# Performance work log

Measured on AMD Instinct MI355X. Metric: run time of the kernel, lower is better.

## Reference

```python
import jax, jax.numpy as jnp
import numpy as np

N = 100000      # nodes
E = 1600000     # edges (avg degree 16)
IN = 128        # in_size
H = 4           # num_heads
DH = 16         # hid_size (per-head)
DO = 16         # out_size (per-head)
NEG_SLOPE = 0.2 # DGL GATConv default leaky_relu slope


def setup_inputs():
    key = jax.random.key(0)
    ks = jax.random.split(key, 12)
    s = 0.1
    return {
        "x":   jax.random.normal(ks[0], (N, IN), jnp.float32),
        "src": jax.random.randint(ks[1], (E,), 0, N, jnp.int32),
        "dst": jax.random.randint(ks[2], (E,), 0, N, jnp.int32),
        # layer 1: in=128 -> H*DH=64, residual Linear (128 != 64)
        "W1":    jax.random.normal(ks[3], (IN, H * DH), jnp.float32) * s,
        "al1":   jax.random.normal(ks[4], (H, DH), jnp.float32) * s,
        "ar1":   jax.random.normal(ks[5], (H, DH), jnp.float32) * s,
        "resW1": jax.random.normal(ks[6], (IN, H * DH), jnp.float32) * s,
        "b1":    jnp.zeros((H * DH,), jnp.float32),
        # layer 2: in=H*DH=64 -> H*DO=64, residual is Identity reshape (64 == 64)
        "W2":  jax.random.normal(ks[7], (H * DH, H * DO), jnp.float32) * s,
        "al2": jax.random.normal(ks[8], (H, DO), jnp.float32) * s,
        "ar2": jax.random.normal(ks[9], (H, DO), jnp.float32) * s,
        "b2":  jnp.zeros((H * DO,), jnp.float32),
    }


def gat_layer(h, W, al, ar, res, bias, src, dst):
    """One DGL-style GATConv (no internal activation). Returns [N, H, D]."""
    d = W.shape[1] // H
    feat = (h @ W).reshape(-1, H, d)                       # [N,H,D]
    el = jnp.einsum('nhd,hd->nh', feat, al)                # [N,H]
    er = jnp.einsum('nhd,hd->nh', feat, ar)                # [N,H]
    e = jax.nn.leaky_relu(el[src] + er[dst], NEG_SLOPE)    # [E,H]
    # segment softmax over incoming edges of each destination node
    emax = jax.lax.stop_gradient(jax.ops.segment_max(e, dst, num_segments=N))
    ee = jnp.exp(e - emax[dst])                            # [E,H]
    den = jax.ops.segment_sum(ee, dst, num_segments=N)     # [N,H]
    alpha = ee / den[dst]                                  # [E,H]
    msg = alpha[:, :, None] * feat[src]                    # [E,H,D]
    out = jax.ops.segment_sum(msg, dst, num_segments=N)    # [N,H,D]
    return out + res + bias.reshape(1, H, d)


def reference(x, src, dst, W1, al1, ar1, resW1, b1, W2, al2, ar2, b2):
    # layer 1 (residual via Linear since IN != H*DH)
    res1 = (x @ resW1).reshape(N, H, DH)
    h = gat_layer(x, W1, al1, ar1, res1, b1, src, dst)     # [N,H,DH]
    h = jax.nn.elu(h.reshape(N, H * DH))                   # flatten + elu (dropout=eval identity)
    # layer 2 (identity residual since H*DH == H*DO)
    res2 = h.reshape(N, H, DO)
    h = gat_layer(h, W2, al2, ar2, res2, b2, src, dst)     # [N,H,DO]
    return h.mean(axis=1)                                  # [N,DO]
```

## Files before the change

### kernel.cpp

```cpp
#include <hip/hip_runtime.h>
#include <hip/hip_bf16.h>

static inline int cdiv(int a, int b){ return (a+b-1)/b; }

#define LEAKY(x) ((x) >= 0.f ? (x) : 0.2f*(x))

#define NBK   512
#define NBKSH 9
#define CAP   12288

__device__ inline unsigned short bf16bits(float f){
  __hip_bfloat16 h = __float2bfloat16(f);
  return *reinterpret_cast<unsigned short*>(&h);
}


__global__ __launch_bounds__(256) void binA(const int* __restrict__ src,
    const int* __restrict__ dst, int* __restrict__ acur, unsigned int* __restrict__ tmp,
    int E, int B, int epb)
{
  __shared__ int cnt1[256], cnt2[256], gbase[256];
  const int tid = threadIdx.x;
  cnt1[tid] = 0; cnt2[tid] = 0;
  __syncthreads();
  const int beg = blockIdx.x*epb, end = min(E, beg+epb);
  for (int e = beg+tid; e < end; e += 256) atomicAdd(&cnt1[dst[e]>>NBKSH], 1);
  __syncthreads();
  if (tid < B) gbase[tid] = atomicAdd(&acur[tid], cnt1[tid]);
  __syncthreads();
  for (int e = beg+tid; e < end; e += 256) {
    int s = src[e], d = dst[e];
    int b = d >> NBKSH;
    int tk = atomicAdd(&cnt2[b], 1);
    int slot = gbase[b] + tk;
    if (slot < CAP)
      tmp[(size_t)b*CAP + slot] = ((unsigned)s << NBKSH) | (unsigned)(d & (NBK-1));
  }
}


__global__ __launch_bounds__(256) void bucket_scan(const int* __restrict__ acur,
    int* __restrict__ bbase, int* __restrict__ off, int B, int N, int E)
{
  __shared__ int wsum[4];
  const int tid = threadIdx.x, lane = tid & 63, wave = tid >> 6;
  int v = (tid < B) ? acur[tid] : 0;
  int x = v;
  #pragma unroll
  for (int s = 1; s < 64; s <<= 1) { int t = __shfl_up(x, s); if (lane >= s) x += t; }
  if (lane == 63) wsum[wave] = x;
  __syncthreads();
  if (tid == 0) { int r = 0; for (int w = 0; w < 4; w++) { int t = wsum[w]; wsum[w] = r; r += t; } }
  __syncthreads();
  int excl = wsum[wave] + x - v;
  if (tid < B)    bbase[tid] = excl;
  if (tid == B-1) bbase[B]   = excl + v;
  if (tid == 0)   off[N]     = E;
}


__global__ __launch_bounds__(256) void binC(const unsigned int* __restrict__ tmp,
    const int* __restrict__ acur, const int* __restrict__ bbase,
    int* __restrict__ off, int* __restrict__ csr_src, int N)
{
  __shared__ int sA[NBK], sB[NBK];
  const int b = blockIdx.x, tid = threadIdx.x;
  const int m = min(acur[b], CAP);
  const int base = bbase[b];
  const int n0 = b*NBK;
  const int nn = min(NBK, N - n0);
  for (int j = tid; j < NBK; j += 256) sA[j] = 0;
  __syncthreads();
  const unsigned int* tb = tmp + (size_t)b*CAP;
  for (int i = tid; i < m; i += 256) atomicAdd(&sA[tb[i] & (NBK-1)], 1);
  __syncthreads();
  int* in = sA; int* ob = sB;
  for (int st = 1; st < NBK; st <<= 1) {
    for (int j = tid; j < NBK; j += 256) { int v = in[j]; if (j >= st) v += in[j-st]; ob[j] = v; }
    __syncthreads();
    int* t = in; in = ob; ob = t;
  }
  for (int j = tid; j < NBK; j += 256) ob[j] = j ? in[j-1] : 0;
  __syncthreads();
  for (int j = tid; j < nn; j += 256) off[n0 + j] = base + ob[j];
  __syncthreads();
  for (int i = tid; i < m; i += 256) {
    unsigned v = tb[i];
    int pos = atomicAdd(&ob[v & (NBK-1)], 1);
    csr_src[base + pos] = (int)(v >> NBKSH);
  }
}


template<bool ATTN, bool BF16OUT>
__global__ __launch_bounds__(256) void lin128(const float* __restrict__ X,
    const float* __restrict__ W, const float* __restrict__ al, const float* __restrict__ ar,
    void* __restrict__ featout, float* __restrict__ el, float* __restrict__ er, int n)
{
  __shared__ float Ws[128*64];
  __shared__ float Xs[32*129];
  const int tid = threadIdx.x;
  const int nbase = blockIdx.x * 32;
  for (int i = tid; i < 128*64/4; i += 256) ((float4*)Ws)[i] = ((const float4*)W)[i];
  for (int idx = tid; idx < 32*32; idx += 256) {
    int node = idx >> 5, fq = idx & 31;
    int gn = nbase + node;
    float4 v = (gn < n) ? ((const float4*)X)[(size_t)gn*32 + fq] : float4{0.f,0.f,0.f,0.f};
    Xs[node*129 + fq*4 + 0] = v.x;
    Xs[node*129 + fq*4 + 1] = v.y;
    Xs[node*129 + fq*4 + 2] = v.z;
    Xs[node*129 + fq*4 + 3] = v.w;
  }
  __syncthreads();
  const int c0 = (tid & 15) * 4;
  const int n0 = (tid >> 4) * 2;
  float a00=0,a01=0,a02=0,a03=0, a10=0,a11=0,a12=0,a13=0;
  #pragma unroll 4
  for (int k = 0; k < 128; k++) {
    float4 w = *(const float4*)&Ws[k*64 + c0];
    float x0 = Xs[n0*129 + k];
    float x1 = Xs[n0*129 + 129 + k];
    a00 = fmaf(x0, w.x, a00); a01 = fmaf(x0, w.y, a01);
    a02 = fmaf(x0, w.z, a02); a03 = fmaf(x0, w.w, a03);
    a10 = fmaf(x1, w.x, a10); a11 = fmaf(x1, w.y, a11);
    a12 = fmaf(x1, w.z, a12); a13 = fmaf(x1, w.w, a13);
  }
  const int g0 = nbase + n0, g1 = g0 + 1;
  if (BF16OUT) {
    unsigned short* fb = (unsigned short*)featout;
    if (g0 < n) *(ushort4*)&fb[(size_t)g0*64 + c0] = ushort4{bf16bits(a00),bf16bits(a01),bf16bits(a02),bf16bits(a03)};
    if (g1 < n) *(ushort4*)&fb[(size_t)g1*64 + c0] = ushort4{bf16bits(a10),bf16bits(a11),bf16bits(a12),bf16bits(a13)};
  } else {
    float* fb = (float*)featout;
    if (g0 < n) *(float4*)&fb[(size_t)g0*64 + c0] = float4{a00,a01,a02,a03};
    if (g1 < n) *(float4*)&fb[(size_t)g1*64 + c0] = float4{a10,a11,a12,a13};
  }
  if (ATTN) {
    float l0=al[c0], l1=al[c0+1], l2=al[c0+2], l3=al[c0+3];
    float r0=ar[c0], r1=ar[c0+1], r2=ar[c0+2], r3=ar[c0+3];
    float e0 = a00*l0 + a01*l1 + a02*l2 + a03*l3;
    float e1 = a10*l0 + a11*l1 + a12*l2 + a13*l3;
    float q0 = a00*r0 + a01*r1 + a02*r2 + a03*r3;
    float q1 = a10*r0 + a11*r1 + a12*r2 + a13*r3;
    e0 += __shfl_xor(e0,1); e0 += __shfl_xor(e0,2);
    e1 += __shfl_xor(e1,1); e1 += __shfl_xor(e1,2);
    q0 += __shfl_xor(q0,1); q0 += __shfl_xor(q0,2);
    q1 += __shfl_xor(q1,1); q1 += __shfl_xor(q1,2);
    if ((tid & 3) == 0) {
      int h = (tid & 15) >> 2;
      if (g0 < n) { el[g0*4+h] = e0; er[g0*4+h] = q0; }
      if (g1 < n) { el[g1*4+h] = e1; er[g1*4+h] = q1; }
    }
  }
}


__global__ __launch_bounds__(256) void lin64(const float* __restrict__ X,
    const float* __restrict__ W, const float* __restrict__ al, const float* __restrict__ ar,
    unsigned short* __restrict__ feat, float* __restrict__ el, float* __restrict__ er, int n)
{
  __shared__ float Ws[64*64];
  __shared__ float Xs[64*65];
  const int tid = threadIdx.x;
  const int nbase = blockIdx.x * 64;
  for (int i = tid; i < 64*64/4; i += 256) ((float4*)Ws)[i] = ((const float4*)W)[i];
  for (int idx = tid; idx < 64*16; idx += 256) {
    int node = idx >> 4, fq = idx & 15;
    int gn = nbase + node;
    float4 v = (gn < n) ? ((const float4*)X)[(size_t)gn*16 + fq] : float4{0.f,0.f,0.f,0.f};
    Xs[node*65 + fq*4 + 0] = v.x;
    Xs[node*65 + fq*4 + 1] = v.y;
    Xs[node*65 + fq*4 + 2] = v.z;
    Xs[node*65 + fq*4 + 3] = v.w;
  }
  __syncthreads();
  const int c0 = (tid & 15) * 4;
  const int n0 = (tid >> 4) * 4;
  float acc[4][4];
  #pragma unroll
  for (int i = 0; i < 4; i++)
    #pragma unroll
    for (int j = 0; j < 4; j++) acc[i][j] = 0.f;
  #pragma unroll 4
  for (int k = 0; k < 64; k++) {
    float4 w = *(const float4*)&Ws[k*64 + c0];
    #pragma unroll
    for (int i = 0; i < 4; i++) {
      float x = Xs[(n0+i)*65 + k];
      acc[i][0] = fmaf(x, w.x, acc[i][0]);
      acc[i][1] = fmaf(x, w.y, acc[i][1]);
      acc[i][2] = fmaf(x, w.z, acc[i][2]);
      acc[i][3] = fmaf(x, w.w, acc[i][3]);
    }
  }
  float l0=al[c0], l1=al[c0+1], l2=al[c0+2], l3=al[c0+3];
  float r0=ar[c0], r1=ar[c0+1], r2=ar[c0+2], r3=ar[c0+3];
  #pragma unroll
  for (int i = 0; i < 4; i++) {
    int g = nbase + n0 + i;
    if (g < n) *(ushort4*)&feat[(size_t)g*64 + c0] =
        ushort4{bf16bits(acc[i][0]),bf16bits(acc[i][1]),bf16bits(acc[i][2]),bf16bits(acc[i][3])};
    float e = acc[i][0]*l0 + acc[i][1]*l1 + acc[i][2]*l2 + acc[i][3]*l3;
    float q = acc[i][0]*r0 + acc[i][1]*r1 + acc[i][2]*r2 + acc[i][3]*r3;
    e += __shfl_xor(e,1); e += __shfl_xor(e,2);
    q += __shfl_xor(q,1); q += __shfl_xor(q,2);
    if ((tid & 3) == 0 && g < n) {
      int h = (tid & 15) >> 2;
      el[g*4+h] = e; er[g*4+h] = q;
    }
  }
}


template<int LAYER>
__global__ __launch_bounds__(256) void aggregate_fused(const int* __restrict__ off,
    const int* __restrict__ csr_src, const float* __restrict__ el, const float* __restrict__ er,
    const __hip_bfloat16* __restrict__ feat, const float* __restrict__ res,
    const float* __restrict__ bias, float* __restrict__ out, int n)
{
  const int wave = threadIdx.x >> 6, lane = threadIdx.x & 63;
  const int node = blockIdx.x*4 + wave;
  if (node >= n) return;
  const int h = lane >> 4;
  const float erh = er[node*4 + h];
  const int beg = off[node], end = off[node+1];
  float d[8], a[8];
  #pragma unroll
  for (int k = 0; k < 8; k++) { d[k] = 0.f; a[k] = 0.f; }
  int i = beg;
  for (; i + 8 <= end; i += 8) {
    int   s[8]; float p[8], f[8];
    #pragma unroll
    for (int k = 0; k < 8; k++) s[k] = csr_src[i+k];
    #pragma unroll
    for (int k = 0; k < 8; k++) p[k] = __expf(LEAKY(el[s[k]*4 + h] + erh));
    #pragma unroll
    for (int k = 0; k < 8; k++) f[k] = __bfloat162float(feat[(size_t)s[k]*64 + lane]);
    #pragma unroll
    for (int k = 0; k < 8; k++) { d[k] += p[k]; a[k] = fmaf(p[k], f[k], a[k]); }
  }
  for (; i < end; i++) {
    int s = csr_src[i];
    float p = __expf(LEAKY(el[s*4 + h] + erh));
    d[0] += p;
    a[0] = fmaf(p, __bfloat162float(feat[(size_t)s*64 + lane]), a[0]);
  }
  float den = ((d[0]+d[1])+(d[2]+d[3])) + ((d[4]+d[5])+(d[6]+d[7]));
  float acc = ((a[0]+a[1])+(a[2]+a[3])) + ((a[4]+a[5])+(a[6]+a[7]));
  float v = (den > 0.f) ? (acc/den) : 0.f;
  v += res[(size_t)node*64 + lane] + bias[lane];
  if (LAYER == 1) {
    v = (v > 0.f) ? v : expm1f(v);
    out[(size_t)node*64 + lane] = v;
  } else {
    v += __shfl_xor(v, 16);
    v += __shfl_xor(v, 32);
    if (lane < 16) out[(size_t)node*16 + lane] = 0.25f*v;
  }
}


extern "C" void kernel_launch(void* const* d_in, const int* in_sizes, int n_in,
                              void* d_out, int out_size, void* d_ws, size_t ws_size,
                              hipStream_t stream)
{
  (void)n_in; (void)out_size; (void)ws_size;
  const float* x   = (const float*)d_in[0];
  const int*   src = (const int*)  d_in[1];
  const int*   dst = (const int*)  d_in[2];
  const float* W1  = (const float*)d_in[3];
  const float* al1 = (const float*)d_in[4];
  const float* ar1 = (const float*)d_in[5];
  const float* rW1 = (const float*)d_in[6];
  const float* b1  = (const float*)d_in[7];
  const float* W2  = (const float*)d_in[8];
  const float* al2 = (const float*)d_in[9];
  const float* ar2 = (const float*)d_in[10];
  const float* b2  = (const float*)d_in[11];
  float* out = (float*)d_out;

  const int N_ = in_sizes[0] / 128;
  const int E_ = in_sizes[1];
  const int B_ = cdiv(N_, NBK);

  char* ws = (char*)d_ws;
  size_t o = 0;
  auto alloc = [&](size_t bytes)->char* {
    char* p = ws + o; o += (bytes + 255) & ~(size_t)255; return p;
  };
  int*   acur    = (int*)  alloc((size_t)B_*4);
  int*   bbase   = (int*)  alloc(((size_t)B_+1)*4);
  int*   off     = (int*)  alloc(((size_t)N_+1)*4);
  unsigned int* tmp = (unsigned int*)alloc((size_t)B_*CAP*4);
  int*   csr_src = (int*)  alloc((size_t)E_*4);
  unsigned short* featb = (unsigned short*)alloc((size_t)N_*64*2);
  float* el      = (float*)alloc((size_t)N_*4*4);
  float* er      = (float*)alloc((size_t)N_*4*4);
  float* hbuf    = (float*)alloc((size_t)N_*64*4);

  hipMemsetAsync(acur, 0, (size_t)B_*4, stream);
  binA<<<256, 256, 0, stream>>>(src, dst, acur, tmp, E_, B_, cdiv(E_,256));
  bucket_scan<<<1, 256, 0, stream>>>(acur, bbase, off, B_, N_, E_);
  binC<<<B_, 256, 0, stream>>>(tmp, acur, bbase, off, csr_src, N_);

  lin128<true,  true ><<<cdiv(N_,32), 256, 0, stream>>>(x, W1,  al1, ar1, featb, el, er, N_);
  lin128<false, false><<<cdiv(N_,32), 256, 0, stream>>>(x, rW1, nullptr, nullptr, hbuf, nullptr, nullptr, N_);
  aggregate_fused<1><<<cdiv(N_,4), 256, 0, stream>>>(off, csr_src, el, er,
      (const __hip_bfloat16*)featb, hbuf, b1, hbuf, N_);

  lin64<<<cdiv(N_,64), 256, 0, stream>>>(hbuf, W2, al2, ar2, featb, el, er, N_);
  aggregate_fused<2><<<cdiv(N_,4), 256, 0, stream>>>(off, csr_src, el, er,
      (const __hip_bfloat16*)featb, hbuf, b2, out, N_);
}
```

Before: 444.6 us.

## Precompute edge attention scores in separate kernel and shrink CSR buckets

Splits the per-edge exp(leaky(el[src]+er[dst])) computation out of the aggregation into a separate edge-parallel score kernel that writes an alpha array. The CSR now stores (src,dst) pairs so the scorer can index er directly. Bucket size drops from 512 to 256 nodes, which doubles the bucket count and resizes the binning kernels. This adds an E*4 float array plus the doubled CSR width in extra memory traffic, plus two more kernel launches, in exchange for taking the gathered el loads and exps off the aggregation's critical path.

```diff
diff --git a/kernel.cpp b/kernel.cpp
--- a/kernel.cpp
+++ b/kernel.cpp
@@ -5,9 +5,9 @@
 
 #define LEAKY(x) ((x) >= 0.f ? (x) : 0.2f*(x))
 
-#define NBK   512
-#define NBKSH 9
-#define CAP   12288
+#define NBK   256
+#define NBKSH 8
+#define CAP   5120
 
 __device__ inline unsigned short bf16bits(float f){
   __hip_bfloat16 h = __float2bfloat16(f);
@@ -19,14 +19,14 @@
     const int* __restrict__ dst, int* __restrict__ acur, unsigned int* __restrict__ tmp,
     int E, int B, int epb)
 {
-  __shared__ int cnt1[256], cnt2[256], gbase[256];
+  __shared__ int cnt1[512], cnt2[512], gbase[512];
   const int tid = threadIdx.x;
-  cnt1[tid] = 0; cnt2[tid] = 0;
+  for (int j = tid; j < 512; j += 256) { cnt1[j] = 0; cnt2[j] = 0; }
   __syncthreads();
   const int beg = blockIdx.x*epb, end = min(E, beg+epb);
   for (int e = beg+tid; e < end; e += 256) atomicAdd(&cnt1[dst[e]>>NBKSH], 1);
   __syncthreads();
-  if (tid < B) gbase[tid] = atomicAdd(&acur[tid], cnt1[tid]);
+  for (int j = tid; j < B; j += 256) gbase[j] = atomicAdd(&acur[j], cnt1[j]);
   __syncthreads();
   for (int e = beg+tid; e < end; e += 256) {
     int s = src[e], d = dst[e];
@@ -39,10 +39,10 @@
 }
 
 
-__global__ __launch_bounds__(256) void bucket_scan(const int* __restrict__ acur,
+__global__ __launch_bounds__(512) void bucket_scan(const int* __restrict__ acur,
     int* __restrict__ bbase, int* __restrict__ off, int B, int N, int E)
 {
-  __shared__ int wsum[4];
+  __shared__ int wsum[8];
   const int tid = threadIdx.x, lane = tid & 63, wave = tid >> 6;
   int v = (tid < B) ? acur[tid] : 0;
   int x = v;
@@ -50,7 +50,7 @@
   for (int s = 1; s < 64; s <<= 1) { int t = __shfl_up(x, s); if (lane >= s) x += t; }
   if (lane == 63) wsum[wave] = x;
   __syncthreads();
-  if (tid == 0) { int r = 0; for (int w = 0; w < 4; w++) { int t = wsum[w]; wsum[w] = r; r += t; } }
+  if (tid == 0) { int r = 0; for (int w = 0; w < 8; w++) { int t = wsum[w]; wsum[w] = r; r += t; } }
   __syncthreads();
   int excl = wsum[wave] + x - v;
   if (tid < B)    bbase[tid] = excl;
@@ -61,7 +61,7 @@
 
 __global__ __launch_bounds__(256) void binC(const unsigned int* __restrict__ tmp,
     const int* __restrict__ acur, const int* __restrict__ bbase,
-    int* __restrict__ off, int* __restrict__ csr_src, int N)
+    int* __restrict__ off, int2* __restrict__ csr, int N)
 {
   __shared__ int sA[NBK], sB[NBK];
   const int b = blockIdx.x, tid = threadIdx.x;
@@ -69,25 +69,26 @@
   const int base = bbase[b];
   const int n0 = b*NBK;
   const int nn = min(NBK, N - n0);
-  for (int j = tid; j < NBK; j += 256) sA[j] = 0;
+  if (tid < NBK) sA[tid] = 0;
   __syncthreads();
   const unsigned int* tb = tmp + (size_t)b*CAP;
   for (int i = tid; i < m; i += 256) atomicAdd(&sA[tb[i] & (NBK-1)], 1);
   __syncthreads();
   int* in = sA; int* ob = sB;
   for (int st = 1; st < NBK; st <<= 1) {
-    for (int j = tid; j < NBK; j += 256) { int v = in[j]; if (j >= st) v += in[j-st]; ob[j] = v; }
+    if (tid < NBK) { int v = in[tid]; if (tid >= st) v += in[tid-st]; ob[tid] = v; }
     __syncthreads();
     int* t = in; in = ob; ob = t;
   }
-  for (int j = tid; j < NBK; j += 256) ob[j] = j ? in[j-1] : 0;
-  __syncthreads();
-  for (int j = tid; j < nn; j += 256) off[n0 + j] = base + ob[j];
+  if (tid < NBK) ob[tid] = tid ? in[tid-1] : 0;
+  __syncthreads();
+  if (tid < nn) off[n0 + tid] = base + ob[tid];
   __syncthreads();
   for (int i = tid; i < m; i += 256) {
     unsigned v = tb[i];
-    int pos = atomicAdd(&ob[v & (NBK-1)], 1);
-    csr_src[base + pos] = (int)(v >> NBKSH);
+    int local = v & (NBK-1);
+    int pos = atomicAdd(&ob[local], 1);
+    csr[base + pos] = int2{(int)(v >> NBKSH), n0 + local};
   }
 }
 
@@ -212,9 +213,22 @@
 }
 
 
+__global__ __launch_bounds__(256) void score_kernel(const int2* __restrict__ csr,
+    const float* __restrict__ el, const float* __restrict__ er,
+    float* __restrict__ alpha, int E4)
+{
+  int t = blockIdx.x*256 + threadIdx.x;
+  if (t >= E4) return;
+  int i = t >> 2, h = t & 3;
+  int2 sd = csr[i];
+  float e = el[sd.x*4 + h] + er[sd.y*4 + h];
+  alpha[t] = __expf(LEAKY(e));
+}
+
+
 template<int LAYER>
 __global__ __launch_bounds__(256) void aggregate_fused(const int* __restrict__ off,
-    const int* __restrict__ csr_src, const float* __restrict__ el, const float* __restrict__ er,
+    const int2* __restrict__ csr, const float* __restrict__ alpha,
     const __hip_bfloat16* __restrict__ feat, const float* __restrict__ res,
     const float* __restrict__ bias, float* __restrict__ out, int n)
 {
@@ -222,7 +236,6 @@
   const int node = blockIdx.x*4 + wave;
   if (node >= n) return;
   const int h = lane >> 4;
-  const float erh = er[node*4 + h];
   const int beg = off[node], end = off[node+1];
   float d[8], a[8];
   #pragma unroll
@@ -231,17 +244,17 @@
   for (; i + 8 <= end; i += 8) {
     int   s[8]; float p[8], f[8];
     #pragma unroll
-    for (int k = 0; k < 8; k++) s[k] = csr_src[i+k];
-    #pragma unroll
-    for (int k = 0; k < 8; k++) p[k] = __expf(LEAKY(el[s[k]*4 + h] + erh));
+    for (int k = 0; k < 8; k++) s[k] = csr[i+k].x;
+    #pragma unroll
+    for (int k = 0; k < 8; k++) p[k] = alpha[(i+k)*4 + h];
     #pragma unroll
     for (int k = 0; k < 8; k++) f[k] = __bfloat162float(feat[(size_t)s[k]*64 + lane]);
     #pragma unroll
     for (int k = 0; k < 8; k++) { d[k] += p[k]; a[k] = fmaf(p[k], f[k], a[k]); }
   }
   for (; i < end; i++) {
-    int s = csr_src[i];
-    float p = __expf(LEAKY(el[s*4 + h] + erh));
+    int s = csr[i].x;
+    float p = alpha[i*4 + h];
     d[0] += p;
     a[0] = fmaf(p, __bfloat162float(feat[(size_t)s*64 + lane]), a[0]);
   }
@@ -292,7 +305,8 @@
   int*   bbase   = (int*)  alloc(((size_t)B_+1)*4);
   int*   off     = (int*)  alloc(((size_t)N_+1)*4);
   unsigned int* tmp = (unsigned int*)alloc((size_t)B_*CAP*4);
-  int*   csr_src = (int*)  alloc((size_t)E_*4);
+  int2*  csr     = (int2*) alloc((size_t)E_*8);
+  float* alpha   = (float*)alloc((size_t)E_*4*4);
   unsigned short* featb = (unsigned short*)alloc((size_t)N_*64*2);
   float* el      = (float*)alloc((size_t)N_*4*4);
   float* er      = (float*)alloc((size_t)N_*4*4);
@@ -300,15 +314,17 @@
 
   hipMemsetAsync(acur, 0, (size_t)B_*4, stream);
   binA<<<256, 256, 0, stream>>>(src, dst, acur, tmp, E_, B_, cdiv(E_,256));
-  bucket_scan<<<1, 256, 0, stream>>>(acur, bbase, off, B_, N_, E_);
-  binC<<<B_, 256, 0, stream>>>(tmp, acur, bbase, off, csr_src, N_);
+  bucket_scan<<<1, 512, 0, stream>>>(acur, bbase, off, B_, N_, E_);
+  binC<<<B_, 256, 0, stream>>>(tmp, acur, bbase, off, csr, N_);
 
   lin128<true,  true ><<<cdiv(N_,32), 256, 0, stream>>>(x, W1,  al1, ar1, featb, el, er, N_);
   lin128<false, false><<<cdiv(N_,32), 256, 0, stream>>>(x, rW1, nullptr, nullptr, hbuf, nullptr, nullptr, N_);
-  aggregate_fused<1><<<cdiv(N_,4), 256, 0, stream>>>(off, csr_src, el, er,
+  score_kernel<<<cdiv(E_*4,256), 256, 0, stream>>>(csr, el, er, alpha, E_*4);
+  aggregate_fused<1><<<cdiv(N_,4), 256, 0, stream>>>(off, csr, alpha,
       (const __hip_bfloat16*)featb, hbuf, b1, hbuf, N_);
 
   lin64<<<cdiv(N_,64), 256, 0, stream>>>(hbuf, W2, al2, ar2, featb, el, er, N_);
-  aggregate_fused<2><<<cdiv(N_,4), 256, 0, stream>>>(off, csr_src, el, er,
+  score_kernel<<<cdiv(E_*4,256), 256, 0, stream>>>(csr, el, er, alpha, E_*4);
+  aggregate_fused<2><<<cdiv(N_,4), 256, 0, stream>>>(off, csr, alpha,
       (const __hip_bfloat16*)featb, hbuf, b2, out, N_);
 }
```

After: 436.5 us. No clear change (-1.8%).
